# Performance work log

Hardware: AMD Instinct MI355X
Metric: run time of the kernel (lower is better)

Reference implementation:

```python
import jax, jax.numpy as jnp
import numpy as np


def setup_inputs() -> dict:
    key = jax.random.key(0)
    ks = jax.random.split(key, 13)
    B, T, D = 512, 256, 64
    H, G = 256, 192          # encoder hidden, lifted dim
    L = D + G                # ldim = 256
    s = lambda n: 1.0 / np.sqrt(n)
    return {
        "x": jax.random.normal(ks[0], (B, T, D), jnp.float32),
        "u": jax.random.normal(ks[1], (B, T, D), jnp.float32),
        "Wx1": jax.random.normal(ks[2], (D, H), jnp.float32) * s(D),
        "bx1": jax.random.normal(ks[3], (H,), jnp.float32) * 0.01,
        "Wx2": jax.random.normal(ks[4], (H, H), jnp.float32) * s(H),
        "bx2": jax.random.normal(ks[5], (H,), jnp.float32) * 0.01,
        "Wx3": jax.random.normal(ks[6], (H, G), jnp.float32) * s(H),
        "Wu1": jax.random.normal(ks[7], (D, H), jnp.float32) * s(D),
        "bu1": jax.random.normal(ks[8], (H,), jnp.float32) * 0.01,
        "Wu2": jax.random.normal(ks[9], (H, G), jnp.float32) * s(H),
        "WB": jax.random.normal(ks[10], (D + G, L), jnp.float32) * s(D + G),
        "WK": jax.random.normal(ks[11], (L, L), jnp.float32) * s(L),
        "bK": jax.random.normal(ks[12], (L,), jnp.float32) * 0.01,
        "n_shifts": 256,
    }


def reference(x, u, Wx1, bx1, Wx2, bx2, Wx3, Wu1, bu1, Wu2, WB, WK, bK, n_shifts):
    x = x[:, :n_shifts, :]
    u = u[:, :n_shifts, :]
    # encoder_x: relu(Linear) -> relu(Linear) -> Linear(no bias), dropout p=0 is identity
    g = jnp.maximum(x @ Wx1 + bx1, 0.0)
    g = jnp.maximum(g @ Wx2 + bx2, 0.0)
    g = g @ Wx3
    y = jnp.concatenate([x, g], axis=-1)          # [B, T, ldim]
    # encoder_u: relu(Linear) -> Linear(no bias)
    v = jnp.maximum(u @ Wu1 + bu1, 0.0) @ Wu2
    uu = jnp.concatenate([u, v], axis=-1)         # [B, T, D+G]
    Bu = uu @ WB                                  # [B, T, ldim]
    # Koopman linear recurrence: y_{t+1} = K y_t + bK + Bu_t
    y0 = y[:, 0, :]                               # [B, ldim]

    def step(carry, bu_t):
        y_next = carry @ WK + bK + bu_t
        return y_next, y_next

    _, ys = jax.lax.scan(step, y0, jnp.swapaxes(Bu[:, :-1, :], 0, 1))  # [T-1, B, ldim]
    y_pred = jnp.concatenate([y0[:, None, :], jnp.swapaxes(ys, 0, 1)], axis=1)
    return (y, y_pred)
```

## Files before the change

### kernel.cpp

```cpp
#include <hip/hip_runtime.h>
#include <hip/hip_bf16.h>

#define MM 131072
#define TILE 64
#define BK 16

typedef __attribute__((ext_vector_type(8))) short short8;
typedef __attribute__((ext_vector_type(4))) float f32x4;

#define GLP(p) (const __attribute__((address_space(1))) void*)(p)
#define LDSP(p) (__attribute__((address_space(3))) void*)(p)

static __device__ __forceinline__ unsigned short f2bf(float f) {
    union { float f; unsigned int u; } v; v.f = f;
    unsigned int r = v.u + 0x7FFF + ((v.u >> 16) & 1);
    return (unsigned short)(r >> 16);
}
static __device__ __forceinline__ float bf2f(unsigned short h) {
    union { float f; unsigned int u; } v; v.u = ((unsigned int)h) << 16;
    return v.f;
}

__global__ __launch_bounds__(256) void conv2_bf16(
    const float* __restrict__ x, const float* __restrict__ u,
    __hip_bfloat16* __restrict__ xb, __hip_bfloat16* __restrict__ ub,
    float* __restrict__ y)
{
    int i = blockIdx.x * 256 + threadIdx.x;
    const float* s; __hip_bfloat16* d; int j; bool isx;
    if (i < 2097152) { s = x; d = xb; j = i; isx = true; }
    else             { s = u; d = ub; j = i - 2097152; isx = false; }
    const float4 v = ((const float4*)s)[j];
    union { unsigned short h[4]; uint2 u2; } p;
    p.h[0] = f2bf(v.x); p.h[1] = f2bf(v.y);
    p.h[2] = f2bf(v.z); p.h[3] = f2bf(v.w);
    ((uint2*)d)[j] = p.u2;
    if (isx) {
        const int r = j >> 4, q = j & 15;
        ((float4*)(y + (size_t)r * 256))[q] = v;
    }
}

__global__ __launch_bounds__(256) void wtrans_all(
    const float* __restrict__ W0, const float* __restrict__ W1,
    const float* __restrict__ W2, const float* __restrict__ W3,
    const float* __restrict__ W4, const float* __restrict__ W5,
    __hip_bfloat16* __restrict__ T0, __hip_bfloat16* __restrict__ T1,
    __hip_bfloat16* __restrict__ T2, __hip_bfloat16* __restrict__ T3,
    __hip_bfloat16* __restrict__ T4, __hip_bfloat16* __restrict__ T5)
{
    const int b = blockIdx.x;
    const float* W; __hip_bfloat16* T; int K, N, i0;
    if      (b < 64)  { W = W0; T = T0; K = 64;  N = 256; i0 = b; }
    else if (b < 320) { W = W1; T = T1; K = 256; N = 256; i0 = b - 64; }
    else if (b < 512) { W = W2; T = T2; K = 256; N = 192; i0 = b - 320; }
    else if (b < 576) { W = W3; T = T3; K = 64;  N = 256; i0 = b - 512; }
    else if (b < 768) { W = W4; T = T4; K = 256; N = 192; i0 = b - 576; }
    else              { W = W5; T = T5; K = 256; N = 256; i0 = b - 768; }
    const int i = i0 * 256 + threadIdx.x;
    if (i < K * N) {
        const int n = i / K, k = i - n * K;
        T[i] = __float2bfloat16(W[(size_t)k * N + n]);
    }
}

template <bool RELU, bool BIAS>
__global__ __launch_bounds__(256) void gemm_ff(
    const float* __restrict__ A, int lda,
    const float* __restrict__ W, int ldw,
    const float* __restrict__ bias,
    float* __restrict__ C, int ldc, int coff,
    int K)
{
    __shared__ __align__(16) float As[BK][TILE + 4];
    __shared__ __align__(16) float Ws[BK][TILE];

    const int tx = threadIdx.x & 15;
    const int ty = threadIdx.x >> 4;
    const int row0 = blockIdx.x * TILE;
    const int col0 = blockIdx.y * TILE;

    float acc[4][4] = {};

    for (int k0 = 0; k0 < K; k0 += BK) {
        {
            const int kk = threadIdx.x & 15;
            const int r  = threadIdx.x >> 4;
            #pragma unroll
            for (int rr = 0; rr < 4; ++rr) {
                const int row = row0 + r + rr * 16;
                As[kk][r + rr * 16] = A[(size_t)row * lda + k0 + kk];
            }
        }
        {
            const int n  = threadIdx.x & 63;
            const int kz = threadIdx.x >> 6;
            #pragma unroll
            for (int kq = 0; kq < 4; ++kq) {
                const int kk = kz + kq * 4;
                Ws[kk][n] = W[(size_t)(k0 + kk) * ldw + col0 + n];
            }
        }
        __syncthreads();
        #pragma unroll
        for (int kk = 0; kk < BK; ++kk) {
            const float4 a4 = *(const float4*)&As[kk][ty * 4];
            const float4 w4 = *(const float4*)&Ws[kk][tx * 4];
            const float av[4] = {a4.x, a4.y, a4.z, a4.w};
            const float wv[4] = {w4.x, w4.y, w4.z, w4.w};
            #pragma unroll
            for (int i = 0; i < 4; ++i)
                #pragma unroll
                for (int j = 0; j < 4; ++j)
                    acc[i][j] += av[i] * wv[j];
        }
        __syncthreads();
    }

    #pragma unroll
    for (int i = 0; i < 4; ++i) {
        const int r = row0 + ty * 4 + i;
        #pragma unroll
        for (int j = 0; j < 4; ++j) {
            const int c = col0 + tx * 4 + j;
            float v = acc[i][j];
            if (BIAS) v += bias[c];
            if (RELU) v = fmaxf(v, 0.0f);
            C[(size_t)r * ldc + coff + c] = v;
        }
    }
}

__global__ __launch_bounds__(256) void bigbt(
    const float* __restrict__ WB, const float* __restrict__ WBW,
    const float* __restrict__ WBW2, const float* __restrict__ WBW3,
    __hip_bfloat16* __restrict__ T4)
{
    const int kk = blockIdx.x;
    const int j = kk >> 8, k = kk & 255;
    const float* src = (j == 0) ? WB : (j == 1) ? WBW : (j == 2) ? WBW2 : WBW3;
    const int n = threadIdx.x;
    ((unsigned short*)T4)[(size_t)n * 1024 + kk] = f2bf(src[(size_t)k * 256 + n]);
}

__global__ __launch_bounds__(256) void ck4k(
    const float* __restrict__ bK, const float* __restrict__ W,
    const float* __restrict__ W2, const float* __restrict__ W3,
    float* __restrict__ cK4)
{
    const int col = threadIdx.x;
    float s = bK[col];
    for (int k = 0; k < 256; ++k)
        s += bK[k] * (W[(size_t)k * 256 + col] + W2[(size_t)k * 256 + col]
                      + W3[(size_t)k * 256 + col]);
    cK4[col] = s;
}

__global__ __launch_bounds__(256) void stashk(
    const __hip_bfloat16* __restrict__ u_bf, const __hip_bfloat16* __restrict__ v,
    const __hip_bfloat16* __restrict__ WBT, const float* __restrict__ bK,
    float* __restrict__ stash)
{
    __shared__ float uuL[3][256];
    const int b = blockIdx.x;
    const int tid = threadIdx.x;
    #pragma unroll
    for (int p = 0; p < 3; ++p) {
        float val;
        if (tid < 64) val = bf2f(((const unsigned short*)u_bf)[((size_t)b * 256 + p) * 64 + tid]);
        else          val = bf2f(((const unsigned short*)v)[((size_t)b * 256 + p) * 192 + tid - 64]);
        uuL[p][tid] = val;
    }
    __syncthreads();
    const int col = tid;
    float a0 = bK[col], a1 = a0, a2 = a0;
    for (int k = 0; k < 256; ++k) {
        const float w = bf2f(((const unsigned short*)WBT)[(size_t)col * 256 + k]);
        a0 += uuL[0][k] * w;
        a1 += uuL[1][k] * w;
        a2 += uuL[2][k] * w;
    }
    stash[((size_t)b * 3 + 0) * 256 + col] = a0;
    stash[((size_t)b * 3 + 1) * 256 + col] = a1;
    stash[((size_t)b * 3 + 2) * 256 + col] = a2;
}

__global__ __launch_bounds__(512) void ffx(
    const __hip_bfloat16* __restrict__ x_bf,
    const __hip_bfloat16* __restrict__ W1T, const float* __restrict__ b1,
    const __hip_bfloat16* __restrict__ W2T, const float* __restrict__ b2,
    const __hip_bfloat16* __restrict__ W3T,
    float* __restrict__ y)
{
    __shared__ __align__(16) __hip_bfloat16 I[128 * 256];
    __shared__ __align__(16) __hip_bfloat16 Bs[256 * 32];
    __shared__ __align__(16) __hip_bfloat16 As[128 * 32];

    const int tid  = threadIdx.x;
    const int lane = tid & 63;
    const int wid  = tid >> 6;
    const int wm   = wid & 1;
    const int wn   = wid >> 1;
    const int row0 = blockIdx.x * 128;
    const int rlow = lane & 15;
    const int c    = lane >> 4;

    f32x4 acc[4][4];

    #pragma unroll
    for (int mi = 0; mi < 4; ++mi)
        #pragma unroll
        for (int ni = 0; ni < 4; ++ni)
            acc[mi][ni] = {0.f, 0.f, 0.f, 0.f};

    for (int k0 = 0; k0 < 64; k0 += 32) {
        {
            const int i = tid;
            const int row = i >> 2;
            const int cl  = (i & 3) ^ ((row >> 1) & 3);
            __builtin_amdgcn_global_load_lds(
                GLP(x_bf + (size_t)(row0 + row) * 64 + k0 + cl * 8),
                LDSP(As + i * 8), 16, 0, 0);
        }
        #pragma unroll
        for (int r = 0; r < 2; ++r) {
            const int i = r * 512 + tid;
            const int row = i >> 2;
            const int cl  = (i & 3) ^ ((row >> 1) & 3);
            __builtin_amdgcn_global_load_lds(
                GLP(W1T + (size_t)row * 64 + k0 + cl * 8),
                LDSP(Bs + i * 8), 16, 0, 0);
        }
        __syncthreads();
        short8 af[4], bfr[4];
        #pragma unroll
        for (int mi = 0; mi < 4; ++mi) {
            const int row  = wm * 64 + mi * 16 + rlow;
            const int phys = c ^ ((row >> 1) & 3);
            af[mi] = *(const short8*)((const char*)As + row * 64 + phys * 16);
        }
        #pragma unroll
        for (int ni = 0; ni < 4; ++ni) {
            const int row  = wn * 64 + ni * 16 + rlow;
            const int phys = c ^ ((row >> 1) & 3);
            bfr[ni] = *(const short8*)((const char*)Bs + row * 64 + phys * 16);
        }
        #pragma unroll
        for (int mi = 0; mi < 4; ++mi)
            #pragma unroll
            for (int ni = 0; ni < 4; ++ni)
                acc[mi][ni] = __builtin_amdgcn_mfma_f32_16x16x32_bf16(
                    af[mi], bfr[ni], acc[mi][ni], 0, 0, 0);
        __syncthreads();
    }
    #pragma unroll
    for (int ni = 0; ni < 4; ++ni) {
        const int col = wn * 64 + ni * 16 + rlow;
        const float bv = b1[col];
        #pragma unroll
        for (int mi = 0; mi < 4; ++mi)
            #pragma unroll
            for (int q = 0; q < 4; ++q) {
                const int row = wm * 64 + mi * 16 + c * 4 + q;
                const int byte = (row * 512 + col * 2) ^ ((row & 7) << 4);
                *(unsigned short*)((char*)I + byte) = f2bf(fmaxf(acc[mi][ni][q] + bv, 0.f));
            }
    }
    __syncthreads();

    #pragma unroll
    for (int mi = 0; mi < 4; ++mi)
        #pragma unroll
        for (int ni = 0; ni < 4; ++ni)
            acc[mi][ni] = {0.f, 0.f, 0.f, 0.f};

    for (int k0 = 0; k0 < 256; k0 += 32) {
        #pragma unroll
        for (int r = 0; r < 2; ++r) {
            const int i = r * 512 + tid;
            const int row = i >> 2;
            const int cl  = (i & 3) ^ ((row >> 1) & 3);
            __builtin_amdgcn_global_load_lds(
                GLP(W2T + (size_t)row * 256 + k0 + cl * 8),
                LDSP(Bs + i * 8), 16, 0, 0);
        }
        __syncthreads();
        short8 af[4], bfr[4];
        #pragma unroll
        for (int mi = 0; mi < 4; ++mi) {
            const int row = wm * 64 + mi * 16 + rlow;
            const int off = (row * 512 + k0 * 2 + c * 16) ^ ((row & 7) << 4);
            af[mi] = *(const short8*)((const char*)I + off);
        }
        #pragma unroll
        for (int ni = 0; ni < 4; ++ni) {
            const int row  = wn * 64 + ni * 16 + rlow;
            const int phys = c ^ ((row >> 1) & 3);
            bfr[ni] = *(const short8*)((const char*)Bs + row * 64 + phys * 16);
        }
        #pragma unroll
        for (int mi = 0; mi < 4; ++mi)
            #pragma unroll
            for (int ni = 0; ni < 4; ++ni)
                acc[mi][ni] = __builtin_amdgcn_mfma_f32_16x16x32_bf16(
                    af[mi], bfr[ni], acc[mi][ni], 0, 0, 0);
        __syncthreads();
    }
    #pragma unroll
    for (int ni = 0; ni < 4; ++ni) {
        const int col = wn * 64 + ni * 16 + rlow;
        const float bv = b2[col];
        #pragma unroll
        for (int mi = 0; mi < 4; ++mi)
            #pragma unroll
            for (int q = 0; q < 4; ++q) {
                const int row = wm * 64 + mi * 16 + c * 4 + q;
                const int byte = (row * 512 + col * 2) ^ ((row & 7) << 4);
                *(unsigned short*)((char*)I + byte) = f2bf(fmaxf(acc[mi][ni][q] + bv, 0.f));
            }
    }
    __syncthreads();

    f32x4 a3[4][3];
    #pragma unroll
    for (int mi = 0; mi < 4; ++mi)
        #pragma unroll
        for (int ni = 0; ni < 3; ++ni)
            a3[mi][ni] = {0.f, 0.f, 0.f, 0.f};

    for (int k0 = 0; k0 < 256; k0 += 32) {
        #pragma unroll
        for (int r = 0; r < 2; ++r) {
            const int i = r * 512 + tid;
            if (i < 768) {
                const int row = i >> 2;
                const int cl  = (i & 3) ^ ((row >> 1) & 3);
                __builtin_amdgcn_global_load_lds(
                    GLP(W3T + (size_t)row * 256 + k0 + cl * 8),
                    LDSP(Bs + i * 8), 16, 0, 0);
            }
        }
        __syncthreads();
        short8 af[4], bfr[3];
        #pragma unroll
        for (int mi = 0; mi < 4; ++mi) {
            const int row = wm * 64 + mi * 16 + rlow;
            const int off = (row * 512 + k0 * 2 + c * 16) ^ ((row & 7) << 4);
            af[mi] = *(const short8*)((const char*)I + off);
        }
        #pragma unroll
        for (int ni = 0; ni < 3; ++ni) {
            const int row  = wn * 48 + ni * 16 + rlow;
            const int phys = c ^ ((row >> 1) & 3);
            bfr[ni] = *(const short8*)((const char*)Bs + row * 64 + phys * 16);
        }
        #pragma unroll
        for (int mi = 0; mi < 4; ++mi)
            #pragma unroll
            for (int ni = 0; ni < 3; ++ni)
                a3[mi][ni] = __builtin_amdgcn_mfma_f32_16x16x32_bf16(
                    af[mi], bfr[ni], a3[mi][ni], 0, 0, 0);
        __syncthreads();
    }
    #pragma unroll
    for (int ni = 0; ni < 3; ++ni) {
        const int col = wn * 48 + ni * 16 + rlow;
        #pragma unroll
        for (int mi = 0; mi < 4; ++mi)
            #pragma unroll
            for (int q = 0; q < 4; ++q) {
                const int row = row0 + wm * 64 + mi * 16 + c * 4 + q;
                y[(size_t)row * 256 + 64 + col] = a3[mi][ni][q];
            }
    }
}

__global__ __launch_bounds__(512) void ffu(
    const __hip_bfloat16* __restrict__ u_bf,
    const __hip_bfloat16* __restrict__ W1T, const float* __restrict__ b1,
    const __hip_bfloat16* __restrict__ W2T,
    __hip_bfloat16* __restrict__ vout)
{
    __shared__ __align__(16) __hip_bfloat16 I[128 * 256];
    __shared__ __align__(16) __hip_bfloat16 Bs[256 * 32];
    __shared__ __align__(16) __hip_bfloat16 As[128 * 32];

    const int tid  = threadIdx.x;
    const int lane = tid & 63;
    const int wid  = tid >> 6;
    const int wm   = wid & 1;
    const int wn   = wid >> 1;
    const int row0 = blockIdx.x * 128;
    const int rlow = lane & 15;
    const int c    = lane >> 4;

    f32x4 acc[4][4];
    #pragma unroll
    for (int mi = 0; mi < 4; ++mi)
        #pragma unroll
        for (int ni = 0; ni < 4; ++ni)
            acc[mi][ni] = {0.f, 0.f, 0.f, 0.f};

    for (int k0 = 0; k0 < 64; k0 += 32) {
        {
            const int i = tid;
            const int row = i >> 2;
            const int cl  = (i & 3) ^ ((row >> 1) & 3);
            __builtin_amdgcn_global_load_lds(
                GLP(u_bf + (size_t)(row0 + row) * 64 + k0 + cl * 8),
                LDSP(As + i * 8), 16, 0, 0);
        }
        #pragma unroll
        for (int r = 0; r < 2; ++r) {
            const int i = r * 512 + tid;
            const int row = i >> 2;
            const int cl  = (i & 3) ^ ((row >> 1) & 3);
            __builtin_amdgcn_global_load_lds(
                GLP(W1T + (size_t)row * 64 + k0 + cl * 8),
                LDSP(Bs + i * 8), 16, 0, 0);
        }
        __syncthreads();
        short8 af[4], bfr[4];
        #pragma unroll
        for (int mi = 0; mi < 4; ++mi) {
            const int row  = wm * 64 + mi * 16 + rlow;
            const int phys = c ^ ((row >> 1) & 3);
            af[mi] = *(const short8*)((const char*)As + row * 64 + phys * 16);
        }
        #pragma unroll
        for (int ni = 0; ni < 4; ++ni) {
            const int row  = wn * 64 + ni * 16 + rlow;
            const int phys = c ^ ((row >> 1) & 3);
            bfr[ni] = *(const short8*)((const char*)Bs + row * 64 + phys * 16);
        }
        #pragma unroll
        for (int mi = 0; mi < 4; ++mi)
            #pragma unroll
            for (int ni = 0; ni < 4; ++ni)
                acc[mi][ni] = __builtin_amdgcn_mfma_f32_16x16x32_bf16(
                    af[mi], bfr[ni], acc[mi][ni], 0, 0, 0);
        __syncthreads();
    }
    #pragma unroll
    for (int ni = 0; ni < 4; ++ni) {
        const int col = wn * 64 + ni * 16 + rlow;
        const float bv = b1[col];
        #pragma unroll
        for (int mi = 0; mi < 4; ++mi)
            #pragma unroll
            for (int q = 0; q < 4; ++q) {
                const int row = wm * 64 + mi * 16 + c * 4 + q;
                const int byte = (row * 512 + col * 2) ^ ((row & 7) << 4);
                *(unsigned short*)((char*)I + byte) = f2bf(fmaxf(acc[mi][ni][q] + bv, 0.f));
            }
    }
    __syncthreads();

    f32x4 a3[4][3];
    #pragma unroll
    for (int mi = 0; mi < 4; ++mi)
        #pragma unroll
        for (int ni = 0; ni < 3; ++ni)
            a3[mi][ni] = {0.f, 0.f, 0.f, 0.f};

    for (int k0 = 0; k0 < 256; k0 += 32) {
        #pragma unroll
        for (int r = 0; r < 2; ++r) {
            const int i = r * 512 + tid;
            if (i < 768) {
                const int row = i >> 2;
                const int cl  = (i & 3) ^ ((row >> 1) & 3);
                __builtin_amdgcn_global_load_lds(
                    GLP(W2T + (size_t)row * 256 + k0 + cl * 8),
                    LDSP(Bs + i * 8), 16, 0, 0);
            }
        }
        __syncthreads();
        short8 af[4], bfr[3];
        #pragma unroll
        for (int mi = 0; mi < 4; ++mi) {
            const int row = wm * 64 + mi * 16 + rlow;
            const int off = (row * 512 + k0 * 2 + c * 16) ^ ((row & 7) << 4);
            af[mi] = *(const short8*)((const char*)I + off);
        }
        #pragma unroll
        for (int ni = 0; ni < 3; ++ni) {
            const int row  = wn * 48 + ni * 16 + rlow;
            const int phys = c ^ ((row >> 1) & 3);
            bfr[ni] = *(const short8*)((const char*)Bs + row * 64 + phys * 16);
        }
        #pragma unroll
        for (int mi = 0; mi < 4; ++mi)
            #pragma unroll
            for (int ni = 0; ni < 3; ++ni)
                a3[mi][ni] = __builtin_amdgcn_mfma_f32_16x16x32_bf16(
                    af[mi], bfr[ni], a3[mi][ni], 0, 0, 0);
        __syncthreads();
    }
    #pragma unroll
    for (int ni = 0; ni < 3; ++ni) {
        const int col = wn * 48 + ni * 16 + rlow;
        #pragma unroll
        for (int mi = 0; mi < 4; ++mi)
            #pragma unroll
            for (int q = 0; q < 4; ++q) {
                const int row = row0 + wm * 64 + mi * 16 + c * 4 + q;
                ((unsigned short*)vout)[(size_t)row * 192 + col] = f2bf(a3[mi][ni][q]);
            }
    }
}

__global__ __launch_bounds__(256) void d4g(
    const __hip_bfloat16* __restrict__ u_bf, const __hip_bfloat16* __restrict__ v,
    const __hip_bfloat16* __restrict__ WBT4, const float* __restrict__ cK4,
    float* __restrict__ yp)
{
    __shared__ __align__(16) __hip_bfloat16 As[132 * 32];
    __shared__ __align__(16) __hip_bfloat16 Bs[4][128 * 32];

    const int tid  = threadIdx.x;
    const int lane = tid & 63;
    const int wid  = tid >> 6;
    const int wm   = wid & 1;
    const int wn   = wid >> 1;
    const int row0 = blockIdx.x * 128;
    const int col0 = blockIdx.y * 128;
    const int rlow = lane & 15;
    const int c    = lane >> 4;

    f32x4 acc[4][4];
    #pragma unroll
    for (int mi = 0; mi < 4; ++mi)
        #pragma unroll
        for (int ni = 0; ni < 4; ++ni)
            acc[mi][ni] = {0.f, 0.f, 0.f, 0.f};

    for (int kl = 0; kl < 256; kl += 32) {
        const __hip_bfloat16* Ab; int Al, kk;
        if (kl < 64) { Ab = u_bf; Al = 64;  kk = kl; }
        else         { Ab = v;    Al = 192; kk = kl - 64; }

        #pragma unroll
        for (int r = 0; r < 3; ++r) {
            const int i = r * 256 + tid;
            if (i < 528) {
                const int row = i >> 2;
                const int cl  = (i & 3) ^ ((row >> 1) & 3);
                int srow = row0 - 4 + row;
                if (srow < 0) srow = 0;
                __builtin_amdgcn_global_load_lds(
                    GLP(Ab + (size_t)srow * Al + kk + cl * 8),
                    LDSP(As + i * 8), 16, 0, 0);
            }
        }
        #pragma unroll
        for (int r = 0; r < 8; ++r) {
            const int i = r * 256 + tid;
            const int j = i >> 9;
            const int s = i & 511;
            const int row = s >> 2;
            const int cl  = (s & 3) ^ ((row >> 1) & 3);
            __builtin_amdgcn_global_load_lds(
                GLP(WBT4 + (size_t)(col0 + row) * 1024 + j * 256 + kl + cl * 8),
                LDSP(&Bs[0][0] + i * 8), 16, 0, 0);
        }
        __syncthreads();

        #pragma unroll
        for (int j = 0; j < 4; ++j) {
            short8 bfr[4];
            #pragma unroll
            for (int ni = 0; ni < 4; ++ni) {
                const int row  = wn * 64 + ni * 16 + rlow;
                const int phys = c ^ ((row >> 1) & 3);
                bfr[ni] = *(const short8*)((const char*)Bs[j] + row * 64 + phys * 16);
            }
            #pragma unroll
            for (int mi = 0; mi < 4; ++mi) {
                const int prow = wm * 64 + mi * 16 + rlow + 3 - j;
                const int phys = c ^ ((prow >> 1) & 3);
                const short8 af = *(const short8*)((const char*)As + prow * 64 + phys * 16);
                #pragma unroll
                for (int ni = 0; ni < 4; ++ni)
                    acc[mi][ni] = __builtin_amdgcn_mfma_f32_16x16x32_bf16(
                        af, bfr[ni], acc[mi][ni], 0, 0, 0);
            }
        }
        __syncthreads();
    }

    const int q4 = lane >> 4;
    #pragma unroll
    for (int ni = 0; ni < 4; ++ni) {
        const int col = col0 + wn * 64 + ni * 16 + rlow;
        const float bv = cK4[col];
        #pragma unroll
        for (int mi = 0; mi < 4; ++mi) {
            #pragma unroll
            for (int q = 0; q < 4; ++q) {
                const int row = row0 + wm * 64 + mi * 16 + q4 * 4 + q;
                if ((row & 255) >= 4)
                    yp[(size_t)row * 256 + col] = acc[mi][ni][q] + bv;
            }
        }
    }
}

static __device__ __forceinline__ void gather_frags(
    const float* __restrict__ M, int col0, int rlow, int kg,
    short8 (&wh)[2][8], short8 (&wl)[2][8])
{
    #pragma unroll
    for (int tile = 0; tile < 2; ++tile) {
        const int col = col0 + tile * 16 + rlow;
        for (int kc = 0; kc < 8; ++kc) {
            const int k0 = kc * 32 + kg * 8;
            short8 h, l;
            for (int i = 0; i < 8; ++i) {
                const float w = M[(size_t)(k0 + i) * 256 + col];
                const unsigned short hb = f2bf(w);
                h[i] = (short)hb;
                l[i] = (short)f2bf(w - bf2f(hb));
            }
            wh[tile][kc] = h;
            wl[tile][kc] = l;
        }
    }
}

__global__ __launch_bounds__(512, 1) void scan4(
    const float* __restrict__ WK, const float* __restrict__ W4,
    const float* __restrict__ stash,
    const float* __restrict__ y, float* __restrict__ yp)
{
    __shared__ __align__(16) __hip_bfloat16 cbuf[2][2][16 * 256];

    const int tid  = threadIdx.x;
    const int lane = tid & 63;
    const int wid  = tid >> 6;
    const int b0   = blockIdx.x * 4;
    const int col0 = wid * 32;
    const int rlow = lane & 15;
    const int kg   = lane >> 4;
    const int rswz = (rlow & 7) << 4;

    #pragma unroll
    for (int e = 0; e < 2; ++e) {
        const int idx = tid * 2 + e;
        const int br  = idx >> 8;
        const int cc  = idx & 255;
        const float v = y[(size_t)(b0 + br) * 65536 + cc];
        yp[(size_t)(b0 + br) * 65536 + cc] = v;
        const unsigned short hb = f2bf(v);
        const unsigned short lb = f2bf(v - bf2f(hb));
        const int byte = (br * 512 + cc * 2) ^ ((br & 7) << 4);
        *(unsigned short*)((char*)&cbuf[0][0][0] + byte) = hb;
        *(unsigned short*)((char*)&cbuf[0][1][0] + byte) = lb;
    }
    __syncthreads();

    short8 wh[2][8], wl[2][8];
    gather_frags(WK, col0, rlow, kg, wh, wl);

    for (int p = 1; p < 4; ++p) {
        f32x4 aHH[2], aHL[2], aLH[2];
        #pragma unroll
        for (int tile = 0; tile < 2; ++tile) {
            aHH[tile] = {0.f, 0.f, 0.f, 0.f};
            aHL[tile] = {0.f, 0.f, 0.f, 0.f};
            aLH[tile] = {0.f, 0.f, 0.f, 0.f};
        }
        const char* hbase = (const char*)&cbuf[0][0][0];
        const char* lbase = (const char*)&cbuf[0][1][0];
        #pragma unroll
        for (int kc = 0; kc < 8; ++kc) {
            const int off = (rlow * 512 + kg * 16 + kc * 64) ^ rswz;
            const short8 ah = *(const short8*)(hbase + off);
            const short8 al = *(const short8*)(lbase + off);
            aHH[0] = __builtin_amdgcn_mfma_f32_16x16x32_bf16(ah, wh[0][kc], aHH[0], 0, 0, 0);
            aHH[1] = __builtin_amdgcn_mfma_f32_16x16x32_bf16(ah, wh[1][kc], aHH[1], 0, 0, 0);
            aHL[0] = __builtin_amdgcn_mfma_f32_16x16x32_bf16(ah, wl[0][kc], aHL[0], 0, 0, 0);
            aHL[1] = __builtin_amdgcn_mfma_f32_16x16x32_bf16(ah, wl[1][kc], aHL[1], 0, 0, 0);
            aLH[0] = __builtin_amdgcn_mfma_f32_16x16x32_bf16(al, wh[0][kc], aLH[0], 0, 0, 0);
            aLH[1] = __builtin_amdgcn_mfma_f32_16x16x32_bf16(al, wh[1][kc], aLH[1], 0, 0, 0);
        }
        __builtin_amdgcn_sched_barrier(0);
        asm volatile("s_waitcnt lgkmcnt(0)" ::: "memory");
        __builtin_amdgcn_s_barrier();
        __builtin_amdgcn_sched_barrier(0);

        if (kg == p - 1) {
            #pragma unroll
            for (int tile = 0; tile < 2; ++tile) {
                const int col = col0 + tile * 16 + rlow;
                #pragma unroll
                for (int q = 0; q < 4; ++q) {
                    const float cv = stash[((size_t)(b0 + q) * 3 + (p - 1)) * 256 + col];
                    const float yv = aHH[tile][q] + aHL[tile][q] + aLH[tile][q] + cv;
                    const int wr = p * 4 + q;
                    const unsigned short hb = f2bf(yv);
                    const unsigned short lb = f2bf(yv - bf2f(hb));
                    const int byte = (wr * 512 + col * 2) ^ ((wr & 7) << 4);
                    *(unsigned short*)((char*)&cbuf[0][0][0] + byte) = hb;
                    *(unsigned short*)((char*)&cbuf[0][1][0] + byte) = lb;
                    yp[(size_t)(b0 + q) * 65536 + (size_t)p * 256 + col] = yv;
                }
            }
        }
        __builtin_amdgcn_sched_barrier(0);
        asm volatile("s_waitcnt lgkmcnt(0)" ::: "memory");
        __builtin_amdgcn_s_barrier();
        __builtin_amdgcn_sched_barrier(0);
    }

    gather_frags(W4, col0, rlow, kg, wh, wl);

    float dv[2][4];
    #pragma unroll
    for (int tile = 0; tile < 2; ++tile) {
        const int col = col0 + tile * 16 + rlow;
        #pragma unroll
        for (int q = 0; q < 4; ++q)
            dv[tile][q] = yp[(size_t)(b0 + q) * 65536 + (size_t)(4 + kg) * 256 + col];
    }

    int cur = 0;
    for (int s = 0; s < 63; ++s) {
        const int tb = 4 + s * 4;

        float dn[2][4];
        if (s < 62) {
            #pragma unroll
            for (int tile = 0; tile < 2; ++tile) {
                const int col = col0 + tile * 16 + rlow;
                #pragma unroll
                for (int q = 0; q < 4; ++q)
                    dn[tile][q] = yp[(size_t)(b0 + q) * 65536
                                     + (size_t)(tb + 4 + kg) * 256 + col];
            }
        }

        f32x4 aHH[2], aHL[2], aLH[2];
        #pragma unroll
        for (int tile = 0; tile < 2; ++tile) {
            aHH[tile] = {0.f, 0.f, 0.f, 0.f};
            aHL[tile] = {0.f, 0.f, 0.f, 0.f};
            aLH[tile] = {0.f, 0.f, 0.f, 0.f};
        }
        const char* hbase = (const char*)&cbuf[cur][0][0];
        const char* lbase = (const char*)&cbuf[cur][1][0];
        #pragma unroll
        for (int kc = 0; kc < 8; ++kc) {
            const int off = (rlow * 512 + kg * 16 + kc * 64) ^ rswz;
            const short8 ah = *(const short8*)(hbase + off);
            const short8 al = *(const short8*)(lbase + off);
            aHH[0] = __builtin_amdgcn_mfma_f32_16x16x32_bf16(ah, wh[0][kc], aHH[0], 0, 0, 0);
            aHH[1] = __builtin_amdgcn_mfma_f32_16x16x32_bf16(ah, wh[1][kc], aHH[1], 0, 0, 0);
            aHL[0] = __builtin_amdgcn_mfma_f32_16x16x32_bf16(ah, wl[0][kc], aHL[0], 0, 0, 0);
            aHL[1] = __builtin_amdgcn_mfma_f32_16x16x32_bf16(ah, wl[1][kc], aHL[1], 0, 0, 0);
            aLH[0] = __builtin_amdgcn_mfma_f32_16x16x32_bf16(al, wh[0][kc], aLH[0], 0, 0, 0);
            aLH[1] = __builtin_amdgcn_mfma_f32_16x16x32_bf16(al, wh[1][kc], aLH[1], 0, 0, 0);
        }

        char* whb = (char*)&cbuf[cur ^ 1][0][0];
        char* wlb = (char*)&cbuf[cur ^ 1][1][0];
        #pragma unroll
        for (int tile = 0; tile < 2; ++tile) {
            const int col = col0 + tile * 16 + rlow;
            #pragma unroll
            for (int q = 0; q < 4; ++q) {
                const int row = kg * 4 + q;
                const float yv = aHH[tile][q] + aHL[tile][q] + aLH[tile][q] + dv[tile][q];
                const unsigned short hb = f2bf(yv);
                const unsigned short lb = f2bf(yv - bf2f(hb));
                const int byte = (row * 512 + col * 2) ^ ((row & 7) << 4);
                *(unsigned short*)(whb + byte) = hb;
                *(unsigned short*)(wlb + byte) = lb;
                yp[(size_t)(b0 + q) * 65536 + (size_t)(tb + kg) * 256 + col] = yv;
            }
        }
        if (s < 62) {
            #pragma unroll
            for (int tile = 0; tile < 2; ++tile)
                #pragma unroll
                for (int q = 0; q < 4; ++q)
                    dv[tile][q] = dn[tile][q];
        }

        __builtin_amdgcn_sched_barrier(0);
        asm volatile("s_waitcnt lgkmcnt(0)" ::: "memory");
        __builtin_amdgcn_s_barrier();
        __builtin_amdgcn_sched_barrier(0);
        cur ^= 1;
    }
}

extern "C" void kernel_launch(void* const* d_in, const int* in_sizes, int n_in,
                              void* d_out, int out_size, void* d_ws, size_t ws_size,
                              hipStream_t stream)
{
    const float* x   = (const float*)d_in[0];
    const float* u   = (const float*)d_in[1];
    const float* Wx1 = (const float*)d_in[2];
    const float* bx1 = (const float*)d_in[3];
    const float* Wx2 = (const float*)d_in[4];
    const float* bx2 = (const float*)d_in[5];
    const float* Wx3 = (const float*)d_in[6];
    const float* Wu1 = (const float*)d_in[7];
    const float* bu1 = (const float*)d_in[8];
    const float* Wu2 = (const float*)d_in[9];
    const float* WB  = (const float*)d_in[10];
    const float* WK  = (const float*)d_in[11];
    const float* bK  = (const float*)d_in[12];

    float* y  = (float*)d_out;
    float* yp = y + (size_t)MM * 256;

    char* ws = (char*)d_ws;
    __hip_bfloat16* x_bf = (__hip_bfloat16*)(ws);
    __hip_bfloat16* u_bf = (__hip_bfloat16*)(ws + 16777216);
    __hip_bfloat16* wTb  = (__hip_bfloat16*)(ws + 33554432);
    __hip_bfloat16* Wx1T = wTb;
    __hip_bfloat16* Wx2T = wTb + 16384;
    __hip_bfloat16* Wx3T = wTb + 81920;
    __hip_bfloat16* Wu1T = wTb + 131072;
    __hip_bfloat16* Wu2T = wTb + 147456;
    __hip_bfloat16* WBT  = wTb + 196608;
    __hip_bfloat16* t2   = (__hip_bfloat16*)(ws + 34078720);
    float* W2f   = (float*)(ws + 101187584);
    float* W3f   = (float*)(ws + 101449728);
    float* W4f   = (float*)(ws + 101711872);
    float* WBWf  = (float*)(ws + 101974016);
    float* WBW2f = (float*)(ws + 102236160);
    float* WBW3f = (float*)(ws + 102498304);
    __hip_bfloat16* WBT4 = (__hip_bfloat16*)(ws + 102760448);
    float* cK4   = (float*)(ws + 103284736);
    float* stash = (float*)(ws + 103285760);

    dim3 blk(256);

    conv2_bf16<<<16384, blk, 0, stream>>>(x, u, x_bf, u_bf, y);
    wtrans_all<<<1024, blk, 0, stream>>>(Wx1, Wx2, Wx3, Wu1, Wu2, WB,
                                         Wx1T, Wx2T, Wx3T, Wu1T, Wu2T, WBT);

    gemm_ff<false, false><<<dim3(4, 4), blk, 0, stream>>>(WK,    256, WK,  256, nullptr, W2f,   256, 0, 256);
    gemm_ff<false, false><<<dim3(4, 4), blk, 0, stream>>>(W2f,   256, WK,  256, nullptr, W3f,   256, 0, 256);
    gemm_ff<false, false><<<dim3(4, 4), blk, 0, stream>>>(W2f,   256, W2f, 256, nullptr, W4f,   256, 0, 256);
    gemm_ff<false, false><<<dim3(4, 4), blk, 0, stream>>>(WB,    256, WK,  256, nullptr, WBWf,  256, 0, 256);
    gemm_ff<false, false><<<dim3(4, 4), blk, 0, stream>>>(WBWf,  256, WK,  256, nullptr, WBW2f, 256, 0, 256);
    gemm_ff<false, false><<<dim3(4, 4), blk, 0, stream>>>(WBW2f, 256, WK,  256, nullptr, WBW3f, 256, 0, 256);
    bigbt<<<1024, blk, 0, stream>>>(WB, WBWf, WBW2f, WBW3f, WBT4);
    ck4k<<<1, blk, 0, stream>>>(bK, WK, W2f, W3f, cK4);

    ffx<<<1024, dim3(512), 0, stream>>>(x_bf, Wx1T, bx1, Wx2T, bx2, Wx3T, y);
    ffu<<<1024, dim3(512), 0, stream>>>(u_bf, Wu1T, bu1, Wu2T, t2);

    stashk<<<512, blk, 0, stream>>>(u_bf, t2, WBT, bK, stash);
    d4g<<<dim3(1024, 2), blk, 0, stream>>>(u_bf, t2, WBT4, cK4, yp);

    scan4<<<128, dim3(512), 0, stream>>>(WK, W4f, stash, y, yp);
}
```

Before: 467.9 us.

## Extend recurrence chunking from 4-step to 8-step with K^8 powers

Changes the Koopman scan decomposition from K^4 stride to K^8 stride. The direct Bu-contribution GEMM now covers 8 lagged terms, and the sequential scan runs 31 steps of 8 rows, two batches per block, over 256 blocks instead of 128. Weight-power precomputation is batched into three grouped GEMM launches that build K^2, K^4, K^8 and WB·K^1..7, replacing six separate launches. This shortens the serial dependency chain and doubles scan parallelism, at the cost of a larger d8g GEMM (K=2048), more bf16 error accumulating through the higher powers, and more precompute.

```diff
diff --git a/kernel.cpp b/kernel.cpp
--- a/kernel.cpp
+++ b/kernel.cpp
@@ -2,8 +2,6 @@
 #include <hip/hip_bf16.h>
 
 #define MM 131072
-#define TILE 64
-#define BK 16
 
 typedef __attribute__((ext_vector_type(8))) short short8;
 typedef __attribute__((ext_vector_type(4))) float f32x4;
@@ -64,33 +62,33 @@
     }
 }
 
-template <bool RELU, bool BIAS>
-__global__ __launch_bounds__(256) void gemm_ff(
-    const float* __restrict__ A, int lda,
-    const float* __restrict__ W, int ldw,
-    const float* __restrict__ bias,
-    float* __restrict__ C, int ldc, int coff,
-    int K)
-{
-    __shared__ __align__(16) float As[BK][TILE + 4];
-    __shared__ __align__(16) float Ws[BK][TILE];
+struct G5 { const float* a[5]; const float* b[5]; float* c[5]; };
+
+__global__ __launch_bounds__(256) void wgemm(G5 P)
+{
+    __shared__ __align__(16) float As[16][68];
+    __shared__ __align__(16) float Ws[16][64];
+
+    const int e  = blockIdx.x >> 4;
+    const int tl = blockIdx.x & 15;
+    const float* A = P.a[e];
+    const float* W = P.b[e];
+    float*       C = P.c[e];
+    const int row0 = (tl >> 2) * 64;
+    const int col0 = (tl & 3) * 64;
 
     const int tx = threadIdx.x & 15;
     const int ty = threadIdx.x >> 4;
-    const int row0 = blockIdx.x * TILE;
-    const int col0 = blockIdx.y * TILE;
 
     float acc[4][4] = {};
 
-    for (int k0 = 0; k0 < K; k0 += BK) {
+    for (int k0 = 0; k0 < 256; k0 += 16) {
         {
             const int kk = threadIdx.x & 15;
             const int r  = threadIdx.x >> 4;
             #pragma unroll
-            for (int rr = 0; rr < 4; ++rr) {
-                const int row = row0 + r + rr * 16;
-                As[kk][r + rr * 16] = A[(size_t)row * lda + k0 + kk];
-            }
+            for (int rr = 0; rr < 4; ++rr)
+                As[kk][r + rr * 16] = A[(size_t)(row0 + r + rr * 16) * 256 + k0 + kk];
         }
         {
             const int n  = threadIdx.x & 63;
@@ -98,12 +96,12 @@
             #pragma unroll
             for (int kq = 0; kq < 4; ++kq) {
                 const int kk = kz + kq * 4;
-                Ws[kk][n] = W[(size_t)(k0 + kk) * ldw + col0 + n];
-            }
-        }
-        __syncthreads();
-        #pragma unroll
-        for (int kk = 0; kk < BK; ++kk) {
+                Ws[kk][n] = W[(size_t)(k0 + kk) * 256 + col0 + n];
+            }
+        }
+        __syncthreads();
+        #pragma unroll
+        for (int kk = 0; kk < 16; ++kk) {
             const float4 a4 = *(const float4*)&As[kk][ty * 4];
             const float4 w4 = *(const float4*)&Ws[kk][tx * 4];
             const float av[4] = {a4.x, a4.y, a4.z, a4.w};
@@ -118,54 +116,49 @@
     }
 
     #pragma unroll
-    for (int i = 0; i < 4; ++i) {
-        const int r = row0 + ty * 4 + i;
-        #pragma unroll
-        for (int j = 0; j < 4; ++j) {
-            const int c = col0 + tx * 4 + j;
-            float v = acc[i][j];
-            if (BIAS) v += bias[c];
-            if (RELU) v = fmaxf(v, 0.0f);
-            C[(size_t)r * ldc + coff + c] = v;
-        }
-    }
-}
-
-__global__ __launch_bounds__(256) void bigbt(
-    const float* __restrict__ WB, const float* __restrict__ WBW,
-    const float* __restrict__ WBW2, const float* __restrict__ WBW3,
-    __hip_bfloat16* __restrict__ T4)
+    for (int i = 0; i < 4; ++i)
+        #pragma unroll
+        for (int j = 0; j < 4; ++j)
+            C[(size_t)(row0 + ty * 4 + i) * 256 + col0 + tx * 4 + j] = acc[i][j];
+}
+
+struct P8 { const float* m[8]; };
+__global__ __launch_bounds__(256) void bigbt8(P8 p, __hip_bfloat16* __restrict__ T8)
 {
     const int kk = blockIdx.x;
     const int j = kk >> 8, k = kk & 255;
-    const float* src = (j == 0) ? WB : (j == 1) ? WBW : (j == 2) ? WBW2 : WBW3;
     const int n = threadIdx.x;
-    ((unsigned short*)T4)[(size_t)n * 1024 + kk] = f2bf(src[(size_t)k * 256 + n]);
-}
-
-__global__ __launch_bounds__(256) void ck4k(
+    ((unsigned short*)T8)[(size_t)n * 2048 + j * 256 + k] = f2bf(p.m[j][(size_t)k * 256 + n]);
+}
+
+__global__ __launch_bounds__(256) void ck8k(
     const float* __restrict__ bK, const float* __restrict__ W,
-    const float* __restrict__ W2, const float* __restrict__ W3,
-    float* __restrict__ cK4)
-{
+    const float* __restrict__ W2, const float* __restrict__ W4,
+    float* __restrict__ cK8)
+{
+    __shared__ float t[256];
     const int col = threadIdx.x;
-    float s = bK[col];
-    for (int k = 0; k < 256; ++k)
-        s += bK[k] * (W[(size_t)k * 256 + col] + W2[(size_t)k * 256 + col]
-                      + W3[(size_t)k * 256 + col]);
-    cK4[col] = s;
-}
-
-__global__ __launch_bounds__(256) void stashk(
+    float v = bK[col];
+    for (int k = 0; k < 256; ++k) v += bK[k] * W[(size_t)k * 256 + col];
+    t[col] = v; __syncthreads();
+    float v2 = v;
+    for (int k = 0; k < 256; ++k) v2 += t[k] * W2[(size_t)k * 256 + col];
+    __syncthreads(); t[col] = v2; __syncthreads();
+    float v3 = v2;
+    for (int k = 0; k < 256; ++k) v3 += t[k] * W4[(size_t)k * 256 + col];
+    cK8[col] = v3;
+}
+
+__global__ __launch_bounds__(256) void stashk7(
     const __hip_bfloat16* __restrict__ u_bf, const __hip_bfloat16* __restrict__ v,
     const __hip_bfloat16* __restrict__ WBT, const float* __restrict__ bK,
     float* __restrict__ stash)
 {
-    __shared__ float uuL[3][256];
+    __shared__ float uuL[7][256];
     const int b = blockIdx.x;
     const int tid = threadIdx.x;
     #pragma unroll
-    for (int p = 0; p < 3; ++p) {
+    for (int p = 0; p < 7; ++p) {
         float val;
         if (tid < 64) val = bf2f(((const unsigned short*)u_bf)[((size_t)b * 256 + p) * 64 + tid]);
         else          val = bf2f(((const unsigned short*)v)[((size_t)b * 256 + p) * 192 + tid - 64]);
@@ -173,16 +166,17 @@
     }
     __syncthreads();
     const int col = tid;
-    float a0 = bK[col], a1 = a0, a2 = a0;
+    float a[7];
+    #pragma unroll
+    for (int p = 0; p < 7; ++p) a[p] = bK[col];
     for (int k = 0; k < 256; ++k) {
         const float w = bf2f(((const unsigned short*)WBT)[(size_t)col * 256 + k]);
-        a0 += uuL[0][k] * w;
-        a1 += uuL[1][k] * w;
-        a2 += uuL[2][k] * w;
-    }
-    stash[((size_t)b * 3 + 0) * 256 + col] = a0;
-    stash[((size_t)b * 3 + 1) * 256 + col] = a1;
-    stash[((size_t)b * 3 + 2) * 256 + col] = a2;
+        #pragma unroll
+        for (int p = 0; p < 7; ++p) a[p] += uuL[p][k] * w;
+    }
+    #pragma unroll
+    for (int p = 0; p < 7; ++p)
+        stash[((size_t)b * 7 + p) * 256 + col] = a[p];
 }
 
 __global__ __launch_bounds__(512) void ffx(
@@ -510,13 +504,13 @@
     }
 }
 
-__global__ __launch_bounds__(256) void d4g(
+__global__ __launch_bounds__(256) void d8g(
     const __hip_bfloat16* __restrict__ u_bf, const __hip_bfloat16* __restrict__ v,
-    const __hip_bfloat16* __restrict__ WBT4, const float* __restrict__ cK4,
+    const __hip_bfloat16* __restrict__ WBT8, const float* __restrict__ cK8,
     float* __restrict__ yp)
 {
-    __shared__ __align__(16) __hip_bfloat16 As[132 * 32];
-    __shared__ __align__(16) __hip_bfloat16 Bs[4][128 * 32];
+    __shared__ __align__(16) __hip_bfloat16 As[136 * 32];
+    __shared__ __align__(16) __hip_bfloat16 Bs[8][128 * 32];
 
     const int tid  = threadIdx.x;
     const int lane = tid & 63;
@@ -543,10 +537,10 @@
         #pragma unroll
         for (int r = 0; r < 3; ++r) {
             const int i = r * 256 + tid;
-            if (i < 528) {
+            if (i < 544) {
                 const int row = i >> 2;
                 const int cl  = (i & 3) ^ ((row >> 1) & 3);
-                int srow = row0 - 4 + row;
+                int srow = row0 - 8 + row;
                 if (srow < 0) srow = 0;
                 __builtin_amdgcn_global_load_lds(
                     GLP(Ab + (size_t)srow * Al + kk + cl * 8),
@@ -554,20 +548,20 @@
             }
         }
         #pragma unroll
-        for (int r = 0; r < 8; ++r) {
+        for (int r = 0; r < 16; ++r) {
             const int i = r * 256 + tid;
             const int j = i >> 9;
             const int s = i & 511;
             const int row = s >> 2;
             const int cl  = (s & 3) ^ ((row >> 1) & 3);
             __builtin_amdgcn_global_load_lds(
-                GLP(WBT4 + (size_t)(col0 + row) * 1024 + j * 256 + kl + cl * 8),
+                GLP(WBT8 + (size_t)(col0 + row) * 2048 + j * 256 + kl + cl * 8),
                 LDSP(&Bs[0][0] + i * 8), 16, 0, 0);
         }
         __syncthreads();
 
         #pragma unroll
-        for (int j = 0; j < 4; ++j) {
+        for (int j = 0; j < 8; ++j) {
             short8 bfr[4];
             #pragma unroll
             for (int ni = 0; ni < 4; ++ni) {
@@ -577,7 +571,7 @@
             }
             #pragma unroll
             for (int mi = 0; mi < 4; ++mi) {
-                const int prow = wm * 64 + mi * 16 + rlow + 3 - j;
+                const int prow = wm * 64 + mi * 16 + rlow + 7 - j;
                 const int phys = c ^ ((prow >> 1) & 3);
                 const short8 af = *(const short8*)((const char*)As + prow * 64 + phys * 16);
                 #pragma unroll
@@ -593,13 +587,13 @@
     #pragma unroll
     for (int ni = 0; ni < 4; ++ni) {
         const int col = col0 + wn * 64 + ni * 16 + rlow;
-        const float bv = cK4[col];
+        const float bv = cK8[col];
         #pragma unroll
         for (int mi = 0; mi < 4; ++mi) {
             #pragma unroll
             for (int q = 0; q < 4; ++q) {
                 const int row = row0 + wm * 64 + mi * 16 + q4 * 4 + q;
-                if ((row & 255) >= 4)
+                if ((row & 255) >= 8)
                     yp[(size_t)row * 256 + col] = acc[mi][ni][q] + bv;
             }
         }
@@ -628,8 +622,8 @@
     }
 }
 
-__global__ __launch_bounds__(512, 1) void scan4(
-    const float* __restrict__ WK, const float* __restrict__ W4,
+__global__ __launch_bounds__(512, 1) void scan8(
+    const float* __restrict__ WK, const float* __restrict__ W8,
     const float* __restrict__ stash,
     const float* __restrict__ y, float* __restrict__ yp)
 {
@@ -638,31 +632,32 @@
     const int tid  = threadIdx.x;
     const int lane = tid & 63;
     const int wid  = tid >> 6;
-    const int b0   = blockIdx.x * 4;
+    const int b0   = blockIdx.x * 2;
     const int col0 = wid * 32;
     const int rlow = lane & 15;
     const int kg   = lane >> 4;
     const int rswz = (rlow & 7) << 4;
 
-    #pragma unroll
-    for (int e = 0; e < 2; ++e) {
-        const int idx = tid * 2 + e;
-        const int br  = idx >> 8;
-        const int cc  = idx & 255;
-        const float v = y[(size_t)(b0 + br) * 65536 + cc];
-        yp[(size_t)(b0 + br) * 65536 + cc] = v;
+    {
+        const int b  = tid >> 8;
+        const int cc = tid & 255;
+        const float v = y[(size_t)(b0 + b) * 65536 + cc];
+        yp[(size_t)(b0 + b) * 65536 + cc] = v;
         const unsigned short hb = f2bf(v);
         const unsigned short lb = f2bf(v - bf2f(hb));
-        const int byte = (br * 512 + cc * 2) ^ ((br & 7) << 4);
+        const int byte = (b * 512 + cc * 2) ^ ((b & 7) << 4);
         *(unsigned short*)((char*)&cbuf[0][0][0] + byte) = hb;
         *(unsigned short*)((char*)&cbuf[0][1][0] + byte) = lb;
+        unsigned int* hz = (unsigned int*)((char*)&cbuf[0][0][0] + 1024);
+        unsigned int* lz = (unsigned int*)((char*)&cbuf[0][1][0] + 1024);
+        for (int i = tid; i < 1792; i += 512) { hz[i] = 0; lz[i] = 0; }
     }
     __syncthreads();
 
     short8 wh[2][8], wl[2][8];
     gather_frags(WK, col0, rlow, kg, wh, wl);
 
-    for (int p = 1; p < 4; ++p) {
+    for (int p = 1; p < 8; ++p) {
         f32x4 aHH[2], aHL[2], aLH[2];
         #pragma unroll
         for (int tile = 0; tile < 2; ++tile) {
@@ -689,21 +684,25 @@
         __builtin_amdgcn_s_barrier();
         __builtin_amdgcn_sched_barrier(0);
 
-        if (kg == p - 1) {
+        const int r0 = 2 * p - 2;
+        if (kg == (r0 >> 2)) {
             #pragma unroll
             for (int tile = 0; tile < 2; ++tile) {
                 const int col = col0 + tile * 16 + rlow;
                 #pragma unroll
                 for (int q = 0; q < 4; ++q) {
-                    const float cv = stash[((size_t)(b0 + q) * 3 + (p - 1)) * 256 + col];
-                    const float yv = aHH[tile][q] + aHL[tile][q] + aLH[tile][q] + cv;
-                    const int wr = p * 4 + q;
-                    const unsigned short hb = f2bf(yv);
-                    const unsigned short lb = f2bf(yv - bf2f(hb));
-                    const int byte = (wr * 512 + col * 2) ^ ((wr & 7) << 4);
-                    *(unsigned short*)((char*)&cbuf[0][0][0] + byte) = hb;
-                    *(unsigned short*)((char*)&cbuf[0][1][0] + byte) = lb;
-                    yp[(size_t)(b0 + q) * 65536 + (size_t)p * 256 + col] = yv;
+                    if ((q >> 1) == ((r0 & 3) >> 1)) {
+                        const int b = q & 1;
+                        const float cv = stash[((size_t)(b0 + b) * 7 + (p - 1)) * 256 + col];
+                        const float yv = aHH[tile][q] + aHL[tile][q] + aLH[tile][q] + cv;
+                        const int wr = 2 * p + b;
+                        const unsigned short hb = f2bf(yv);
+                        const unsigned short lb = f2bf(yv - bf2f(hb));
+                        const int byte = (wr * 512 + col * 2) ^ ((wr & 7) << 4);
+                        *(unsigned short*)((char*)&cbuf[0][0][0] + byte) = hb;
+                        *(unsigned short*)((char*)&cbuf[0][1][0] + byte) = lb;
+                        yp[(size_t)(b0 + b) * 65536 + (size_t)p * 256 + col] = yv;
+                    }
                 }
             }
         }
@@ -713,7 +712,7 @@
         __builtin_amdgcn_sched_barrier(0);
     }
 
-    gather_frags(W4, col0, rlow, kg, wh, wl);
+    gather_frags(W8, col0, rlow, kg, wh, wl);
 
     float dv[2][4];
     #pragma unroll
@@ -721,22 +720,23 @@
         const int col = col0 + tile * 16 + rlow;
         #pragma unroll
         for (int q = 0; q < 4; ++q)
-            dv[tile][q] = yp[(size_t)(b0 + q) * 65536 + (size_t)(4 + kg) * 256 + col];
+            dv[tile][q] = yp[(size_t)(b0 + (q & 1)) * 65536
+                             + (size_t)(8 + kg * 2 + (q >> 1)) * 256 + col];
     }
 
     int cur = 0;
-    for (int s = 0; s < 63; ++s) {
-        const int tb = 4 + s * 4;
+    for (int s = 0; s < 31; ++s) {
+        const int tb = 8 + s * 8;
 
         float dn[2][4];
-        if (s < 62) {
+        if (s < 30) {
             #pragma unroll
             for (int tile = 0; tile < 2; ++tile) {
                 const int col = col0 + tile * 16 + rlow;
                 #pragma unroll
                 for (int q = 0; q < 4; ++q)
-                    dn[tile][q] = yp[(size_t)(b0 + q) * 65536
-                                     + (size_t)(tb + 4 + kg) * 256 + col];
+                    dn[tile][q] = yp[(size_t)(b0 + (q & 1)) * 65536
+                                     + (size_t)(tb + 8 + kg * 2 + (q >> 1)) * 256 + col];
             }
         }
 
@@ -776,10 +776,11 @@
                 const int byte = (row * 512 + col * 2) ^ ((row & 7) << 4);
                 *(unsigned short*)(whb + byte) = hb;
                 *(unsigned short*)(wlb + byte) = lb;
-                yp[(size_t)(b0 + q) * 65536 + (size_t)(tb + kg) * 256 + col] = yv;
-            }
-        }
-        if (s < 62) {
+                yp[(size_t)(b0 + (row & 1)) * 65536
+                   + (size_t)(tb + (row >> 1)) * 256 + col] = yv;
+            }
+        }
+        if (s < 30) {
             #pragma unroll
             for (int tile = 0; tile < 2; ++tile)
                 #pragma unroll
@@ -828,14 +829,18 @@
     __hip_bfloat16* WBT  = wTb + 196608;
     __hip_bfloat16* t2   = (__hip_bfloat16*)(ws + 34078720);
     float* W2f   = (float*)(ws + 101187584);
-    float* W3f   = (float*)(ws + 101449728);
-    float* W4f   = (float*)(ws + 101711872);
+    float* W4f   = (float*)(ws + 101449728);
+    float* W8f   = (float*)(ws + 101711872);
     float* WBWf  = (float*)(ws + 101974016);
     float* WBW2f = (float*)(ws + 102236160);
     float* WBW3f = (float*)(ws + 102498304);
-    __hip_bfloat16* WBT4 = (__hip_bfloat16*)(ws + 102760448);
-    float* cK4   = (float*)(ws + 103284736);
-    float* stash = (float*)(ws + 103285760);
+    float* WBW4f = (float*)(ws + 102760448);
+    float* WBW5f = (float*)(ws + 103022592);
+    float* WBW6f = (float*)(ws + 103284736);
+    float* WBW7f = (float*)(ws + 103546880);
+    __hip_bfloat16* WBT8 = (__hip_bfloat16*)(ws + 103809024);
+    float* cK8   = (float*)(ws + 104857600);
+    float* stash = (float*)(ws + 104858624);
 
     dim3 blk(256);
 
@@ -843,20 +848,31 @@
     wtrans_all<<<1024, blk, 0, stream>>>(Wx1, Wx2, Wx3, Wu1, Wu2, WB,
                                          Wx1T, Wx2T, Wx3T, Wu1T, Wu2T, WBT);
 
-    gemm_ff<false, false><<<dim3(4, 4), blk, 0, stream>>>(WK,    256, WK,  256, nullptr, W2f,   256, 0, 256);
-    gemm_ff<false, false><<<dim3(4, 4), blk, 0, stream>>>(W2f,   256, WK,  256, nullptr, W3f,   256, 0, 256);
-    gemm_ff<false, false><<<dim3(4, 4), blk, 0, stream>>>(W2f,   256, W2f, 256, nullptr, W4f,   256, 0, 256);
-    gemm_ff<false, false><<<dim3(4, 4), blk, 0, stream>>>(WB,    256, WK,  256, nullptr, WBWf,  256, 0, 256);
-    gemm_ff<false, false><<<dim3(4, 4), blk, 0, stream>>>(WBWf,  256, WK,  256, nullptr, WBW2f, 256, 0, 256);
-    gemm_ff<false, false><<<dim3(4, 4), blk, 0, stream>>>(WBW2f, 256, WK,  256, nullptr, WBW3f, 256, 0, 256);
-    bigbt<<<1024, blk, 0, stream>>>(WB, WBWf, WBW2f, WBW3f, WBT4);
-    ck4k<<<1, blk, 0, stream>>>(bK, WK, W2f, W3f, cK4);
+    {
+        G5 L1 = {{WK, WB, nullptr, nullptr, nullptr},
+                 {WK, WK, nullptr, nullptr, nullptr},
+                 {W2f, WBWf, nullptr, nullptr, nullptr}};
+        wgemm<<<32, blk, 0, stream>>>(L1);
+        G5 L2 = {{W2f, WB, WBWf, nullptr, nullptr},
+                 {W2f, W2f, W2f, nullptr, nullptr},
+                 {W4f, WBW2f, WBW3f, nullptr, nullptr}};
+        wgemm<<<48, blk, 0, stream>>>(L2);
+        G5 L3 = {{W4f, WB, WBWf, WBW2f, WBW3f},
+                 {W4f, W4f, W4f, W4f, W4f},
+                 {W8f, WBW4f, WBW5f, WBW6f, WBW7f}};
+        wgemm<<<80, blk, 0, stream>>>(L3);
+    }
+    {
+        P8 p = {{WB, WBWf, WBW2f, WBW3f, WBW4f, WBW5f, WBW6f, WBW7f}};
+        bigbt8<<<2048, blk, 0, stream>>>(p, WBT8);
+    }
+    ck8k<<<1, blk, 0, stream>>>(bK, WK, W2f, W4f, cK8);
 
     ffx<<<1024, dim3(512), 0, stream>>>(x_bf, Wx1T, bx1, Wx2T, bx2, Wx3T, y);
     ffu<<<1024, dim3(512), 0, stream>>>(u_bf, Wu1T, bu1, Wu2T, t2);
 
-    stashk<<<512, blk, 0, stream>>>(u_bf, t2, WBT, bK, stash);
-    d4g<<<dim3(1024, 2), blk, 0, stream>>>(u_bf, t2, WBT4, cK4, yp);
-
-    scan4<<<128, dim3(512), 0, stream>>>(WK, W4f, stash, y, yp);
-}
+    stashk7<<<512, blk, 0, stream>>>(u_bf, t2, WBT, bK, stash);
+    d8g<<<dim3(1024, 2), blk, 0, stream>>>(u_bf, t2, WBT8, cK8, yp);
+
+    scan8<<<256, dim3(512), 0, stream>>>(WK, W8f, stash, y, yp);
+}
```

Result: slower. 567.8 us (+21.4%).
